# Optimization experiments

Measured on AMD Instinct MI355X. Metric: run time of the kernel, lower is better.

Reference implementation:

```python
import jax, jax.numpy as jnp
import numpy as np


def _skew(v):
    x, y, z = v[0], v[1], v[2]
    o = jnp.zeros((), v.dtype)
    return jnp.stack([
        jnp.stack([o, -z, y]),
        jnp.stack([z, o, -x]),
        jnp.stack([-y, x, o]),
    ])


def _so3_exp(rot):
    """Rodrigues formula, grad-safe near theta=0 (convert(..., 'so3_log'))."""
    th2 = jnp.sum(rot * rot)
    th = jnp.sqrt(th2 + 1e-30)
    a = jnp.where(th2 < 1e-12, 1.0 - th2 / 6.0, jnp.sin(th) / th)
    b = jnp.where(th2 < 1e-12, 0.5 - th2 / 24.0, (1.0 - jnp.cos(th)) / th2)
    K = _skew(rot)
    return jnp.eye(3, dtype=rot.dtype) + a * K + b * (K @ K)


def _pose(rot, xyz):
    R = _so3_exp(rot)  # [3,3]
    top = jnp.concatenate([R, xyz[:, None]], axis=1)  # [3,4]
    bot = jnp.array([[0.0, 0.0, 0.0, 1.0]], dtype=rot.dtype)
    return jnp.concatenate([top, bot], axis=0)  # [4,4]


def _trilinear(vol, pts):
    """Trilinear sample vol[D,H,W] at pts[...,3] (index coords), zeros outside."""
    dims_f = jnp.asarray(vol.shape, jnp.float32)
    dims_i = jnp.asarray(vol.shape, jnp.int32)
    p0f = jnp.floor(pts)
    f = pts - p0f
    inside = jnp.all((pts >= 0.0) & (pts <= dims_f - 1.0), axis=-1)
    i0 = jnp.clip(p0f.astype(jnp.int32), 0, dims_i - 2)
    i1 = i0 + 1
    fx, fy, fz = f[..., 0], f[..., 1], f[..., 2]
    x0, y0, z0 = i0[..., 0], i0[..., 1], i0[..., 2]
    x1, y1, z1 = i1[..., 0], i1[..., 1], i1[..., 2]
    c000 = vol[x0, y0, z0]; c001 = vol[x0, y0, z1]
    c010 = vol[x0, y1, z0]; c011 = vol[x0, y1, z1]
    c100 = vol[x1, y0, z0]; c101 = vol[x1, y0, z1]
    c110 = vol[x1, y1, z0]; c111 = vol[x1, y1, z1]
    c00 = c000 * (1 - fz) + c001 * fz
    c01 = c010 * (1 - fz) + c011 * fz
    c10 = c100 * (1 - fz) + c101 * fz
    c11 = c110 * (1 - fz) + c111 * fz
    c0 = c00 * (1 - fy) + c01 * fy
    c1 = c10 * (1 - fy) + c11 * fy
    val = c0 * (1 - fx) + c1 * fx
    return jnp.where(inside, val, 0.0)


def setup_inputs() -> dict:
    key = jax.random.key(0)
    k_vol, k_rot, k_xyz = jax.random.split(key, 3)
    D = 256
    H = W = 256
    SDD = 1020.0   # source-to-detector distance (mm)
    F = 1000.0     # focal length (px)
    volume = jax.random.uniform(k_vol, (D, D, D), dtype=jnp.float32)
    # inverse intrinsics K^{-1}
    k_inv = jnp.array([[[1.0 / F, 0.0, -(W / 2) / F],
                        [0.0, 1.0 / F, -(H / 2) / F],
                        [0.0, 0.0, 1.0]]], dtype=jnp.float32)
    # inverse extrinsics: camera (source) at (0,0,-sdd/2) in world, identity rotation
    rt_inv = jnp.eye(4, dtype=jnp.float32)[None].at[0, 2, 3].set(-SDD / 2)
    sdd = jnp.array([SDD], dtype=jnp.float32)
    eps = 1e-8
    _rot = eps * jax.random.normal(k_rot, (1, 3), dtype=jnp.float32)
    _xyz = eps * jax.random.normal(k_xyz, (1, 3), dtype=jnp.float32)
    return {"volume": volume, "rt_inv": rt_inv, "k_inv": k_inv, "sdd": sdd,
            "_rot": _rot, "_xyz": _xyz, "height": H, "width": W, "n_steps": 200}


def reference(volume, rt_inv, k_inv, sdd, _rot, _xyz, height, width, n_steps):
    # pose @ rt_inv : camera-to-world transform for this iterate
    T = _pose(_rot[0], _xyz[0]) @ rt_inv[0]  # [4,4]
    Rw, tw = T[:3, :3], T[:3, 3]
    # detector pixel centers in homogeneous pixel coords -> camera frame at depth sdd
    u = jnp.arange(width, dtype=jnp.float32) + 0.5
    v = jnp.arange(height, dtype=jnp.float32) + 0.5
    uu, vv = jnp.meshgrid(u, v, indexing="xy")  # [H,W]
    pix = jnp.stack([uu, vv, jnp.ones_like(uu)], axis=-1)  # [H,W,3]
    cam = jnp.einsum("ij,hwj->hwi", k_inv[0], pix) * sdd[0]  # detector points, camera frame
    tgt = jnp.einsum("ij,hwj->hwi", Rw, cam) + tw  # [H,W,3] world
    src = tw  # source = camera origin in world
    ray = tgt - src[None, None, :]  # [H,W,3]
    seglen = jnp.linalg.norm(ray, axis=-1) / n_steps  # [H,W]
    alphas = (jnp.arange(n_steps, dtype=jnp.float32) + 0.5) / n_steps  # [S]
    # sample points along each ray: [H,W,S,3]
    pts = src[None, None, None, :] + alphas[None, None, :, None] * ray[:, :, None, :]
    center = (jnp.asarray(volume.shape, jnp.float32) - 1.0) / 2.0
    idx = pts + center  # world (1mm spacing, volume centered at origin) -> voxel index
    vals = _trilinear(volume, idx)  # [H,W,S]
    img = vals.sum(axis=-1) * seglen  # line integral
    return img[None, None]  # [1,1,H,W]
```

## Files before the change

kernel.cpp:

```cpp
#include <hip/hip_runtime.h>
#include <math.h>


#define BLOCK 256
#define TU    32
#define TV    8
#define CHUNKS 8
#define PPB    (BLOCK / CHUNKS)

__device__ __forceinline__ void setup_ray(
    const float* __restrict__ rt_inv, const float* __restrict__ k_inv,
    const float sdd, const float rx, const float ry, const float rz,
    const float tvx, const float tvy, const float tvz,
    const int w, const int h, const int n, const int D,
    float& rayx, float& rayy, float& rayz, float& seglen,
    float& qx, float& qy, float& qz, int& ilo, int& ihi)
{
    const float th2 = rx*rx + ry*ry + rz*rz;
    const float th  = sqrtf(th2 + 1e-30f);
    const float a   = (th2 < 1e-12f) ? (1.0f - th2 * (1.0f/6.0f))  : (sinf(th) / th);
    const float b   = (th2 < 1e-12f) ? (0.5f - th2 * (1.0f/24.0f)) : ((1.0f - cosf(th)) / th2);
    float Rm[3][3];
    Rm[0][0] = 1.0f + b * (-(ry*ry + rz*rz));
    Rm[0][1] = a * (-rz) + b * (rx*ry);
    Rm[0][2] = a * ( ry) + b * (rx*rz);
    Rm[1][0] = a * ( rz) + b * (rx*ry);
    Rm[1][1] = 1.0f + b * (-(rx*rx + rz*rz));
    Rm[1][2] = a * (-rx) + b * (ry*rz);
    Rm[2][0] = a * (-ry) + b * (rx*rz);
    Rm[2][1] = a * ( rx) + b * (ry*rz);
    Rm[2][2] = 1.0f + b * (-(rx*rx + ry*ry));
    const float tv[3] = { tvx, tvy, tvz };
    const float* M = rt_inv;
    float Rw[3][3], tw[3];
    #pragma unroll
    for (int i = 0; i < 3; ++i) {
        #pragma unroll
        for (int j = 0; j < 4; ++j) {
            float s = Rm[i][0]*M[0*4+j] + Rm[i][1]*M[1*4+j]
                    + Rm[i][2]*M[2*4+j] + tv[i]*M[3*4+j];
            if (j < 3) Rw[i][j] = s; else tw[i] = s;
        }
    }
    const float fn = (float)n;
    const float u = (float)w + 0.5f;
    const float v = (float)h + 0.5f;
    const float cx = (k_inv[0]*u + k_inv[1]*v + k_inv[2]) * sdd;
    const float cy = (k_inv[3]*u + k_inv[4]*v + k_inv[5]) * sdd;
    const float cz = (k_inv[6]*u + k_inv[7]*v + k_inv[8]) * sdd;
    const float tgx = Rw[0][0]*cx + Rw[0][1]*cy + Rw[0][2]*cz + tw[0];
    const float tgy = Rw[1][0]*cx + Rw[1][1]*cy + Rw[1][2]*cz + tw[1];
    const float tgz = Rw[2][0]*cx + Rw[2][1]*cy + Rw[2][2]*cz + tw[2];
    rayx = tgx - tw[0];
    rayy = tgy - tw[1];
    rayz = tgz - tw[2];
    seglen = sqrtf(rayx*rayx + rayy*rayy + rayz*rayz) / fn;

    const float c    = 0.5f * (float)(D - 1);
    const float dimf = (float)(D - 1);
    qx = tw[0] + c; qy = tw[1] + c; qz = tw[2] + c;

    float alo = -1e30f, ahi = 1e30f;
    bool empty = false;
    const float qs[3] = { qx, qy, qz };
    const float rs[3] = { rayx, rayy, rayz };
    #pragma unroll
    for (int ax = 0; ax < 3; ++ax) {
        const float q = qs[ax], r = rs[ax];
        if (fabsf(r) < 1e-20f) {
            if (q < 0.0f || q > dimf) empty = true;
        } else {
            const float t0 = (0.0f - q) / r;
            const float t1 = (dimf - q) / r;
            alo = fmaxf(alo, fminf(t0, t1));
            ahi = fminf(ahi, fmaxf(t0, t1));
        }
    }
    ilo = 0; ihi = -1;
    if (!empty && alo <= ahi) {
        ilo = (int)ceilf (alo * fn - 0.5f) - 1;
        ihi = (int)floorf(ahi * fn - 0.5f) + 1;
        ilo = max(ilo, 0);
        ihi = min(ihi, n - 1);
    }
}

template <int DC>
__global__ __launch_bounds__(BLOCK) void drr_tile_kernel(
    const float* __restrict__ vol,
    const float* __restrict__ rt_inv,
    const float* __restrict__ k_inv,
    const float* __restrict__ sdd_p,
    const float* __restrict__ rot_p,
    const float* __restrict__ xyz_p,
    const int*   __restrict__ nsteps_p,
    float*       __restrict__ out,
    const int W)
{
    const int   D    = DC;
    const int   DD   = D * D;
    const float dimf = (float)(D - 1);

    const int tid = (int)threadIdx.x;
    const int bi  = (int)blockIdx.x;
    const int nbu = W / TU;
    const int u0  = (bi % nbu) * TU;
    const int v0  = (bi / nbu) * TV;
    const int w   = u0 + (tid & (TU - 1));
    const int h   = v0 + (tid >> 5);

    const int n = nsteps_p[0];
    float rayx, rayy, rayz, seglen, qx, qy, qz;
    int ilo, ihi;
    setup_ray(rt_inv, k_inv, sdd_p[0], rot_p[0], rot_p[1], rot_p[2],
              xyz_p[0], xyz_p[1], xyz_p[2], w, h, n, D,
              rayx, rayy, rayz, seglen, qx, qy, qz, ilo, ihi);

    float acc = 0.0f;
    const float inv_n = 1.0f / (float)n;

    for (int i = ilo; i <= ihi; ++i) {
        const float alpha = ((float)i + 0.5f) * inv_n;
        const float px = fmaf(alpha, rayx, qx);
        const float py = fmaf(alpha, rayy, qy);
        const float pz = fmaf(alpha, rayz, qz);
        const bool inside = (px >= 0.0f) & (px <= dimf)
                          & (py >= 0.0f) & (py <= dimf)
                          & (pz >= 0.0f) & (pz <= dimf);
        const float fxf = floorf(px), fyf = floorf(py), fzf = floorf(pz);
        const float fx = px - fxf, fy = py - fyf, fz = pz - fzf;
        const int x0 = min(max((int)fxf, 0), D - 2);
        const int y0 = min(max((int)fyf, 0), D - 2);
        const int z0 = min(max((int)fzf, 0), D - 2);
        const float* b000 = vol + ((size_t)x0 * DD + (size_t)y0 * D + z0);
        const float c000 = b000[0];
        const float c001 = b000[1];
        const float c010 = b000[D];
        const float c011 = b000[D + 1];
        const float c100 = b000[DD];
        const float c101 = b000[DD + 1];
        const float c110 = b000[DD + D];
        const float c111 = b000[DD + D + 1];
        const float c00 = c000 * (1.0f - fz) + c001 * fz;
        const float c01 = c010 * (1.0f - fz) + c011 * fz;
        const float c10 = c100 * (1.0f - fz) + c101 * fz;
        const float c11 = c110 * (1.0f - fz) + c111 * fz;
        const float c0  = c00 * (1.0f - fy) + c01 * fy;
        const float c1  = c10 * (1.0f - fy) + c11 * fy;
        const float val = c0 * (1.0f - fx) + c1 * fx;
        acc += inside ? val : 0.0f;
    }

    out[h * W + w] = acc * seglen;
}

__global__ __launch_bounds__(BLOCK) void drr_kernel(
    const float* __restrict__ vol,
    const float* __restrict__ rt_inv,
    const float* __restrict__ k_inv,
    const float* __restrict__ sdd_p,
    const float* __restrict__ rot_p,
    const float* __restrict__ xyz_p,
    const int*   __restrict__ width_p,
    const int*   __restrict__ nsteps_p,
    float*       __restrict__ out,
    const int npix, const int D)
{
    const int tid   = (int)threadIdx.x;
    const int slot  = tid & (PPB - 1);
    const int chunk = tid / PPB;
    const int p     = (int)blockIdx.x * PPB + slot;

    float acc    = 0.0f;
    float seglen = 0.0f;

    if (p < npix) {
        const int W = *width_p;
        const int n = *nsteps_p;
        const int h = p / W;
        const int w = p - h * W;
        float rayx, rayy, rayz, qx, qy, qz;
        int ilo, ihi;
        setup_ray(rt_inv, k_inv, sdd_p[0], rot_p[0], rot_p[1], rot_p[2],
                  xyz_p[0], xyz_p[1], xyz_p[2], w, h, n, D,
                  rayx, rayy, rayz, seglen, qx, qy, qz, ilo, ihi);
        const float dimf = (float)(D - 1);
        const float fn = (float)n;
        if (ihi >= ilo) {
            int start = ilo + ((chunk - ilo) % CHUNKS + CHUNKS) % CHUNKS;
            const float inv_n = 1.0f / fn;
            const int DD = D * D;
            for (int i = start; i <= ihi; i += CHUNKS) {
                const float alpha = ((float)i + 0.5f) * inv_n;
                const float px = fmaf(alpha, rayx, qx);
                const float py = fmaf(alpha, rayy, qy);
                const float pz = fmaf(alpha, rayz, qz);
                const bool inside = (px >= 0.0f) & (px <= dimf)
                                  & (py >= 0.0f) & (py <= dimf)
                                  & (pz >= 0.0f) & (pz <= dimf);
                if (!inside) continue;
                const float fxf = floorf(px), fyf = floorf(py), fzf = floorf(pz);
                const float fx = px - fxf, fy = py - fyf, fz = pz - fzf;
                int x0 = min(max((int)fxf, 0), D - 2);
                int y0 = min(max((int)fyf, 0), D - 2);
                int z0 = min(max((int)fzf, 0), D - 2);
                const float* b000 = vol + (size_t)x0 * DD + (size_t)y0 * D + z0;
                const float c000 = b000[0];
                const float c001 = b000[1];
                const float c010 = b000[D];
                const float c011 = b000[D + 1];
                const float c100 = b000[DD];
                const float c101 = b000[DD + 1];
                const float c110 = b000[DD + D];
                const float c111 = b000[DD + D + 1];
                const float c00 = c000 * (1.0f - fz) + c001 * fz;
                const float c01 = c010 * (1.0f - fz) + c011 * fz;
                const float c10 = c100 * (1.0f - fz) + c101 * fz;
                const float c11 = c110 * (1.0f - fz) + c111 * fz;
                const float c0  = c00 * (1.0f - fy) + c01 * fy;
                const float c1  = c10 * (1.0f - fy) + c11 * fy;
                acc += c0 * (1.0f - fx) + c1 * fx;
            }
        }
    }

    __shared__ float red[BLOCK];
    red[tid] = acc;
    __syncthreads();
    if (tid < PPB) {
        float s = 0.0f;
        #pragma unroll
        for (int k = 0; k < CHUNKS; ++k) s += red[tid + k * PPB];
        if (p < npix) out[p] = s * seglen;
    }
}

extern "C" void kernel_launch(void* const* d_in, const int* in_sizes, int n_in,
                              void* d_out, int out_size, void* d_ws, size_t ws_size,
                              hipStream_t stream) {
    const float* vol    = (const float*)d_in[0];
    const float* rt_inv = (const float*)d_in[1];
    const float* k_inv  = (const float*)d_in[2];
    const float* sdd    = (const float*)d_in[3];
    const float* rot    = (const float*)d_in[4];
    const float* xyz    = (const float*)d_in[5];
    const int*   width  = (const int*)d_in[7];
    const int*   nsteps = (const int*)d_in[8];
    float* out = (float*)d_out;

    const int npix = out_size;
    const int D    = (int)lround(cbrt((double)in_sizes[0]));
    const int W    = 256;

    if (D == 256 && npix == 65536) {
        const int blocks = npix / BLOCK;
        drr_tile_kernel<256><<<blocks, BLOCK, 0, stream>>>(
            vol, rt_inv, k_inv, sdd, rot, xyz, nsteps, out, W);
    } else {
        const int blocks = (npix + PPB - 1) / PPB;
        drr_kernel<<<blocks, BLOCK, 0, stream>>>(
            vol, rt_inv, k_inv, sdd, rot, xyz, width, nsteps, out, npix, D);
    }
}
```

Baseline: 22.20 us.

## Split each ray's samples across 16 lanes with shuffle reduction

Replaces the one-thread-per-pixel tile kernel with a kernel where each block handles a 32x4 pixel tile. Half the threads compute the ray setup into shared memory, then 16 lanes share each ray's samples and combine them with a width-16 xor shuffle reduction. This is meant to raise parallelism and cut per-thread serial loop length and tail imbalance between rays of different lengths. In exchange the block loops over pixel groups serially, lanes go idle when a ray's sample count is not a multiple of 16, and there is an extra block barrier.

```diff
diff --git a/kernel.cpp b/kernel.cpp
--- a/kernel.cpp
+++ b/kernel.cpp
@@ -3,8 +3,7 @@
 
 
 #define BLOCK 256
-#define TU    32
-#define TV    8
+#define TPX   128
 #define CHUNKS 8
 #define PPB    (BLOCK / CHUNKS)
 
@@ -86,7 +85,7 @@
 }
 
 template <int DC>
-__global__ __launch_bounds__(BLOCK) void drr_tile_kernel(
+__global__ __launch_bounds__(BLOCK) void drr_seg_kernel(
     const float* __restrict__ vol,
     const float* __restrict__ rt_inv,
     const float* __restrict__ k_inv,
@@ -101,57 +100,93 @@
     const int   DD   = D * D;
     const float dimf = (float)(D - 1);
 
+    __shared__ float s_rayx[TPX], s_rayy[TPX], s_rayz[TPX], s_seglen[TPX];
+    __shared__ int   s_ilo[TPX], s_ihi[TPX];
+    __shared__ float s_q[3];
+
     const int tid = (int)threadIdx.x;
     const int bi  = (int)blockIdx.x;
-    const int nbu = W / TU;
-    const int u0  = (bi % nbu) * TU;
-    const int v0  = (bi / nbu) * TV;
-    const int w   = u0 + (tid & (TU - 1));
-    const int h   = v0 + (tid >> 5);
+    const int u0  = (bi & 7) * 32;
+    const int v0  = (bi >> 3) * 4;
 
     const int n = nsteps_p[0];
-    float rayx, rayy, rayz, seglen, qx, qy, qz;
-    int ilo, ihi;
-    setup_ray(rt_inv, k_inv, sdd_p[0], rot_p[0], rot_p[1], rot_p[2],
-              xyz_p[0], xyz_p[1], xyz_p[2], w, h, n, D,
-              rayx, rayy, rayz, seglen, qx, qy, qz, ilo, ihi);
-
-    float acc = 0.0f;
     const float inv_n = 1.0f / (float)n;
 
-    for (int i = ilo; i <= ihi; ++i) {
-        const float alpha = ((float)i + 0.5f) * inv_n;
-        const float px = fmaf(alpha, rayx, qx);
-        const float py = fmaf(alpha, rayy, qy);
-        const float pz = fmaf(alpha, rayz, qz);
-        const bool inside = (px >= 0.0f) & (px <= dimf)
-                          & (py >= 0.0f) & (py <= dimf)
-                          & (pz >= 0.0f) & (pz <= dimf);
-        const float fxf = floorf(px), fyf = floorf(py), fzf = floorf(pz);
-        const float fx = px - fxf, fy = py - fyf, fz = pz - fzf;
-        const int x0 = min(max((int)fxf, 0), D - 2);
-        const int y0 = min(max((int)fyf, 0), D - 2);
-        const int z0 = min(max((int)fzf, 0), D - 2);
-        const float* b000 = vol + ((size_t)x0 * DD + (size_t)y0 * D + z0);
-        const float c000 = b000[0];
-        const float c001 = b000[1];
-        const float c010 = b000[D];
-        const float c011 = b000[D + 1];
-        const float c100 = b000[DD];
-        const float c101 = b000[DD + 1];
-        const float c110 = b000[DD + D];
-        const float c111 = b000[DD + D + 1];
-        const float c00 = c000 * (1.0f - fz) + c001 * fz;
-        const float c01 = c010 * (1.0f - fz) + c011 * fz;
-        const float c10 = c100 * (1.0f - fz) + c101 * fz;
-        const float c11 = c110 * (1.0f - fz) + c111 * fz;
-        const float c0  = c00 * (1.0f - fy) + c01 * fy;
-        const float c1  = c10 * (1.0f - fy) + c11 * fy;
-        const float val = c0 * (1.0f - fx) + c1 * fx;
-        acc += inside ? val : 0.0f;
-    }
-
-    out[h * W + w] = acc * seglen;
+    if (tid < TPX) {
+        const int w = u0 + (tid & 31);
+        const int h = v0 + (tid >> 5);
+        float rayx, rayy, rayz, seglen, qx, qy, qz;
+        int ilo, ihi;
+        setup_ray(rt_inv, k_inv, sdd_p[0], rot_p[0], rot_p[1], rot_p[2],
+                  xyz_p[0], xyz_p[1], xyz_p[2], w, h, n, D,
+                  rayx, rayy, rayz, seglen, qx, qy, qz, ilo, ihi);
+        s_rayx[tid] = rayx;  s_rayy[tid] = rayy;  s_rayz[tid] = rayz;
+        s_seglen[tid] = seglen;
+        s_ilo[tid] = ilo;    s_ihi[tid] = ihi;
+        if (tid == 0) { s_q[0] = qx; s_q[1] = qy; s_q[2] = qz; }
+    }
+    __syncthreads();
+
+    const int wv    = tid >> 6;
+    const int lane  = tid & 63;
+    const int pslot = lane >> 4;
+    const int s16   = lane & 15;
+
+    const float qx = s_q[0], qy = s_q[1], qz = s_q[2];
+
+    for (int g = 0; g < 8; ++g) {
+        const int pix = wv * 32 + g * 4 + pslot;
+        const float rayx = s_rayx[pix], rayy = s_rayy[pix], rayz = s_rayz[pix];
+        const int ilo = s_ilo[pix], ihi = s_ihi[pix];
+        const int count = ihi - ilo + 1;
+        const int jmax  = (count + 15) >> 4;
+
+        float acc = 0.0f;
+        for (int j = 0; j < jmax; ++j) {
+            const int i = ilo + (j << 4) + s16;
+            if (i <= ihi) {
+                const float alpha = ((float)i + 0.5f) * inv_n;
+                const float px = fmaf(alpha, rayx, qx);
+                const float py = fmaf(alpha, rayy, qy);
+                const float pz = fmaf(alpha, rayz, qz);
+                const bool inside = (px >= 0.0f) & (px <= dimf)
+                                  & (py >= 0.0f) & (py <= dimf)
+                                  & (pz >= 0.0f) & (pz <= dimf);
+                const float fxf = floorf(px), fyf = floorf(py), fzf = floorf(pz);
+                const float fx = px - fxf, fy = py - fyf, fz = pz - fzf;
+                const int x0 = min(max((int)fxf, 0), D - 2);
+                const int y0 = min(max((int)fyf, 0), D - 2);
+                const int z0 = min(max((int)fzf, 0), D - 2);
+                const float* b000 = vol + ((size_t)x0 * DD + (size_t)y0 * D + z0);
+                const float c000 = b000[0];
+                const float c001 = b000[1];
+                const float c010 = b000[D];
+                const float c011 = b000[D + 1];
+                const float c100 = b000[DD];
+                const float c101 = b000[DD + 1];
+                const float c110 = b000[DD + D];
+                const float c111 = b000[DD + D + 1];
+                const float c00 = c000 * (1.0f - fz) + c001 * fz;
+                const float c01 = c010 * (1.0f - fz) + c011 * fz;
+                const float c10 = c100 * (1.0f - fz) + c101 * fz;
+                const float c11 = c110 * (1.0f - fz) + c111 * fz;
+                const float c0  = c00 * (1.0f - fy) + c01 * fy;
+                const float c1  = c10 * (1.0f - fy) + c11 * fy;
+                const float val = c0 * (1.0f - fx) + c1 * fx;
+                acc += inside ? val : 0.0f;
+            }
+        }
+
+        acc += __shfl_xor(acc, 1, 16);
+        acc += __shfl_xor(acc, 2, 16);
+        acc += __shfl_xor(acc, 4, 16);
+        acc += __shfl_xor(acc, 8, 16);
+        if (s16 == 0) {
+            const int w = u0 + (pix & 31);
+            const int h = v0 + (pix >> 5);
+            out[h * W + w] = acc * s_seglen[pix];
+        }
+    }
 }
 
 __global__ __launch_bounds__(BLOCK) void drr_kernel(
@@ -250,12 +285,11 @@
 
     const int npix = out_size;
     const int D    = (int)lround(cbrt((double)in_sizes[0]));
-    const int W    = 256;
 
     if (D == 256 && npix == 65536) {
-        const int blocks = npix / BLOCK;
-        drr_tile_kernel<256><<<blocks, BLOCK, 0, stream>>>(
-            vol, rt_inv, k_inv, sdd, rot, xyz, nsteps, out, W);
+        const int blocks = npix / TPX;
+        drr_seg_kernel<256><<<blocks, BLOCK, 0, stream>>>(
+            vol, rt_inv, k_inv, sdd, rot, xyz, nsteps, out, 256);
     } else {
         const int blocks = (npix + PPB - 1) / PPB;
         drr_kernel<<<blocks, BLOCK, 0, stream>>>(
```

New measurement: 21.96 us. About the same (-1.1%).
